# Kernel tuning notes

Measured on AMD Instinct MI355X. Metric: run time of the kernel, lower is better.

Reference implementation:

```python
import jax, jax.numpy as jnp
import numpy as np

HID = 256
E = 2 * HID  # 512, attention embed dim
H = 2        # attention heads


def _lin(x, w, b):
    return x @ w.T + b


def setup_inputs() -> dict:
    key = jax.random.key(0)
    ks = jax.random.split(key, 16)
    N, Ng, G = 65536, 4096, 16
    s = 0.02
    def w(k, o, i):
        return jax.random.normal(k, (o, i), jnp.float32) * s
    return {
        "flat_pair_enc": jax.random.normal(ks[0], (N, E), jnp.float32),
        "flat_pair_encA": jax.random.normal(ks[1], (N, E + 2), jnp.float32),
        "attn_in_w": w(ks[2], 3 * E, E), "attn_in_b": jnp.zeros(3 * E, jnp.float32),
        "attn_out_w": w(ks[3], E, E), "attn_out_b": jnp.zeros(E, jnp.float32),
        "phi1_w1": w(ks[4], HID, E + 2), "phi1_b1": jnp.zeros(HID, jnp.float32),
        "phi1_w2": w(ks[5], HID, HID), "phi1_b2": jnp.zeros(HID, jnp.float32),
        "phi1_w3": w(ks[6], HID, HID), "phi1_b3": jnp.zeros(HID, jnp.float32),
        "phi1_w4": w(ks[7], E, HID), "phi1_b4": jnp.zeros(E, jnp.float32),
        "g_w1": w(ks[8], HID, E), "g_b1": jnp.zeros(HID, jnp.float32),
        "g_w2": w(ks[9], HID, HID), "g_b2": jnp.zeros(HID, jnp.float32),
        "g_w3": w(ks[10], HID, HID), "g_b3": jnp.zeros(HID, jnp.float32),
        "g_w4": w(ks[11], 1, HID), "g_b4": jnp.zeros(1, jnp.float32),
        "phi2_w1": w(ks[12], HID, E), "phi2_b1": jnp.zeros(HID, jnp.float32),
        "phi2_w2": w(ks[13], HID, HID), "phi2_b2": jnp.zeros(HID, jnp.float32),
        "phi2_w3": w(ks[14], 2, HID), "phi2_b3": jnp.zeros(2, jnp.float32),
        "num_groups": 4096,
        "group_size": 16,
    }


def reference(flat_pair_enc, flat_pair_encA,
              attn_in_w, attn_in_b, attn_out_w, attn_out_b,
              phi1_w1, phi1_b1, phi1_w2, phi1_b2, phi1_w3, phi1_b3, phi1_w4, phi1_b4,
              g_w1, g_b1, g_w2, g_b2, g_w3, g_b3, g_w4, g_b4,
              phi2_w1, phi2_b1, phi2_w2, phi2_b2, phi2_w3, phi2_b3,
              num_groups, group_size):
    elu = jax.nn.elu
    Ng, G = num_groups, group_size
    # phi1 (note the double ELU after the second Linear, as in the source)
    h = elu(_lin(flat_pair_encA, phi1_w1, phi1_b1))
    h = elu(elu(_lin(h, phi1_w2, phi1_b2)))
    h = elu(_lin(h, phi1_w3, phi1_b3))
    key1 = _lin(h, phi1_w4, phi1_b4)                      # (N, E)
    x = key1.reshape(Ng, G, E)                            # segmented groups
    # per-group MultiheadAttention (torch semantics: packed in_proj, scale 1/sqrt(dh))
    qkv = x @ attn_in_w.T + attn_in_b                     # (Ng, G, 3E)
    q, k, v = jnp.split(qkv, 3, axis=-1)
    dh = E // H
    def heads(t):
        return t.reshape(Ng, G, H, dh).transpose(0, 2, 1, 3)  # (Ng, H, G, dh)
    q, k, v = heads(q), heads(k), heads(v)
    scores = jnp.einsum('nhqd,nhkd->nhqk', q, k) / jnp.sqrt(jnp.float32(dh))
    a = jax.nn.softmax(scores, axis=-1)
    o = jnp.einsum('nhqk,nhkd->nhqd', a, v).transpose(0, 2, 1, 3).reshape(Ng, G, E)
    key1_mean = (o @ attn_out_w.T + attn_out_b).mean(axis=1)  # (Ng, E) — mean over seq
    # g head
    hg = elu(_lin(key1_mean, g_w1, g_b1))
    hg = elu(_lin(hg, g_w2, g_b2))
    hg = elu(_lin(hg, g_w3, g_b3))
    q_jt = _lin(hg, g_w4, g_b4)                           # (Ng, 1)
    # alt values: k2 + kbar1 - key1/|g|  (counts per group == G)
    alt_val = flat_pair_enc.reshape(Ng, G, E) + key1_mean[:, None, :] - x / G
    hp = elu(_lin(alt_val, phi2_w1, phi2_b1))
    hp = elu(_lin(hp, phi2_w2, phi2_b2))
    alt_q = _lin(hp, phi2_w3, phi2_b3)                    # (Ng, G, 2)
    return (q_jt, alt_q)
```

## Files before the change

### kernel.cpp

```cpp
#include <hip/hip_runtime.h>
#include <cstdint>

typedef __bf16 bf16;
typedef __attribute__((ext_vector_type(8))) __bf16 bf16x8;
typedef __attribute__((ext_vector_type(4))) __bf16 bf16x4;
typedef __attribute__((ext_vector_type(4))) float f32x4;
typedef __attribute__((ext_vector_type(2))) float f32x2;

static __device__ __forceinline__ float elu1(float x) {
    return x > 0.f ? x : (__expf(x) - 1.f);
}

static __device__ __forceinline__ void gl_lds16(const void* gp, void* lp) {
    __builtin_amdgcn_global_load_lds(
        (const __attribute__((address_space(1))) void*)(uintptr_t)gp,
        (__attribute__((address_space(3))) void*)(uint32_t)(uintptr_t)lp,
        16, 0, 0);
}

struct CvtArgs {
    const float* src[13];
    int rows[13];
    int scols[13];
    int dcols[13];
    int total;
};

__global__ void cvt_k(CvtArgs a, bf16* __restrict__ dst) {
    int idx = blockIdx.x * 256 + threadIdx.x;
    if (idx >= a.total) return;
    int rem = idx;
#pragma unroll 1
    for (int s = 0; s < 13; ++s) {
        int sz = a.rows[s] * a.dcols[s];
        if (rem < sz) {
            int r = rem / a.dcols[s];
            int c = rem - r * a.dcols[s];
            float v = (c < a.scols[s]) ? a.src[s][(long)r * a.scols[s] + c] : 0.f;
            dst[idx] = (bf16)v;
            return;
        }
        rem -= sz;
    }
}

struct GemmArgs {
    const float* Af;
    const bf16*  Ab;
    long lda;
    const float* enc;
    const float* km;
    const bf16*  key1;
    const bf16*  W;
    long ldw;
    const float* bias;
    bf16*  Cb;
    float* Cf;
    long ldc;
    int nK;
    int klim;
};

enum { AM_F32 = 0, AM_F32U = 1, AM_BF16 = 2, AM_ALT = 3 };
enum { ACT_NONE = 0, ACT_ELU = 1, ACT_ELU2 = 2 };

template <int AMODE, int ACT, bool OUTB>
__global__ __launch_bounds__(256, 2) void gemm_t(GemmArgs g) {
    __shared__ bf16 As[128 * 64];
    __shared__ bf16 Bs[128 * 64];

    const int tid  = threadIdx.x;
    const int wave = tid >> 6;
    const int lane = tid & 63;
    const int ln   = lane & 15;
    const int quad = lane >> 4;

    const long m0 = (long)blockIdx.x * 128;
    const long n0 = (long)blockIdx.y * 128;
    const int  wm = (wave & 1) * 64;
    const int  wn = (wave >> 1) * 64;

    f32x4 acc[4][4] = {};

    for (int ks = 0; ks < g.nK; ++ks) {
        const int k0 = ks * 64;
        __syncthreads();

        if constexpr (AMODE == AM_BF16) {
            const int cbase = wave * 256;
#pragma unroll
            for (int r = 0; r < 4; ++r) {
                const int c = cbase + r * 64 + lane;
                const int m = c >> 3, s = c & 7;
                const int pg = (s - m) & 7;
                gl_lds16(g.Ab + (m0 + m) * g.lda + k0 + pg * 8, &As[c * 8]);
            }
        } else {
#pragma unroll
            for (int r = 0; r < 4; ++r) {
                const int c = r * 256 + tid;
                const int m = c >> 3, s = c & 7;
                const int pg = (s - m) & 7;
                const int kk = k0 + pg * 8;
                bf16x8 t;
                if constexpr (AMODE == AM_F32) {
                    const float* ap = g.Af + (m0 + m) * g.lda + kk;
                    f32x4 p0 = *(const f32x4*)ap;
                    f32x4 p1 = *(const f32x4*)(ap + 4);
                    t[0] = (bf16)p0.x; t[1] = (bf16)p0.y; t[2] = (bf16)p0.z; t[3] = (bf16)p0.w;
                    t[4] = (bf16)p1.x; t[5] = (bf16)p1.y; t[6] = (bf16)p1.z; t[7] = (bf16)p1.w;
                } else if constexpr (AMODE == AM_F32U) {
                    const float* ap = g.Af + (m0 + m) * g.lda;
                    if (kk + 8 <= g.klim) {
#pragma unroll
                        for (int e = 0; e < 8; e += 2) {
                            f32x2 p = *(const f32x2*)(ap + kk + e);
                            t[e] = (bf16)p.x; t[e + 1] = (bf16)p.y;
                        }
                    } else {
#pragma unroll
                        for (int e = 0; e < 8; ++e) {
                            const int col = kk + e;
                            t[e] = (bf16)(col < g.klim ? ap[col] : 0.f);
                        }
                    }
                } else {
                    const long row = m0 + m;
                    const float* ep = g.enc + row * 512 + kk;
                    const float* mp = g.km + (row >> 4) * 512 + kk;
                    const bf16*  xp = g.key1 + row * 512 + kk;
                    f32x4 e0 = *(const f32x4*)ep;
                    f32x4 e1 = *(const f32x4*)(ep + 4);
                    f32x4 q0 = *(const f32x4*)mp;
                    f32x4 q1 = *(const f32x4*)(mp + 4);
                    bf16x8 x8 = *(const bf16x8*)xp;
                    t[0] = (bf16)(e0.x + q0.x - (float)x8[0] * 0.0625f);
                    t[1] = (bf16)(e0.y + q0.y - (float)x8[1] * 0.0625f);
                    t[2] = (bf16)(e0.z + q0.z - (float)x8[2] * 0.0625f);
                    t[3] = (bf16)(e0.w + q0.w - (float)x8[3] * 0.0625f);
                    t[4] = (bf16)(e1.x + q1.x - (float)x8[4] * 0.0625f);
                    t[5] = (bf16)(e1.y + q1.y - (float)x8[5] * 0.0625f);
                    t[6] = (bf16)(e1.z + q1.z - (float)x8[6] * 0.0625f);
                    t[7] = (bf16)(e1.w + q1.w - (float)x8[7] * 0.0625f);
                }
                *(bf16x8*)(&As[m * 64 + s * 8]) = t;
            }
        }

        {
            const int cbase = wave * 256;
#pragma unroll
            for (int r = 0; r < 4; ++r) {
                const int c = cbase + r * 64 + lane;
                const int n = c >> 3, s = c & 7;
                const int pg = (s - n) & 7;
                gl_lds16(g.W + (n0 + n) * g.ldw + k0 + pg * 8, &Bs[c * 8]);
            }
        }
        __syncthreads();

#pragma unroll
        for (int ksub = 0; ksub < 2; ++ksub) {
            bf16x8 av[4], bv[4];
#pragma unroll
            for (int t = 0; t < 4; ++t) {
                const int m = wm + t * 16 + ln;
                const int sa = ((ksub * 4 + quad) + m) & 7;
                av[t] = *(const bf16x8*)(&As[m * 64 + sa * 8]);
                const int n = wn + t * 16 + ln;
                const int sb = ((ksub * 4 + quad) + n) & 7;
                bv[t] = *(const bf16x8*)(&Bs[n * 64 + sb * 8]);
            }
#pragma unroll
            for (int i = 0; i < 4; ++i)
#pragma unroll
                for (int j = 0; j < 4; ++j)
                    acc[i][j] = __builtin_amdgcn_mfma_f32_16x16x32_bf16(
                        av[i], bv[j], acc[i][j], 0, 0, 0);
        }
    }

#pragma unroll
    for (int i = 0; i < 4; ++i) {
        const long rb = m0 + wm + i * 16 + quad * 4;
#pragma unroll
        for (int j = 0; j < 4; ++j) {
            const long n = n0 + wn + j * 16 + ln;
            const float bvs = g.bias[n];
#pragma unroll
            for (int r = 0; r < 4; ++r) {
                float v = acc[i][j][r] + bvs;
                if constexpr (ACT >= ACT_ELU) v = elu1(v);
                if constexpr (ACT == ACT_ELU2) v = elu1(v);
                const long o = (rb + r) * g.ldc + n;
                if constexpr (OUTB) g.Cb[o] = (bf16)v;
                else                g.Cf[o] = v;
            }
        }
    }
}

__global__ __launch_bounds__(256) void attn_k(const bf16* __restrict__ qkv,
                                              bf16* __restrict__ obar,
                                              int ngroups) {
    const int tid = blockIdx.x * 256 + threadIdx.x;
    const int wv = tid >> 6;
    const int g  = wv >> 1;
    const int h  = wv & 1;
    if (g >= ngroups) return;
    const int lane = threadIdx.x & 63;
    const int i  = lane & 15;
    const int jb = (lane >> 4) << 2;

    const bf16* base  = qkv + (long)g * 16 * 1536;
    const bf16* qrow  = base + (long)i * 1536 + h * 256;
    const bf16* kbase = base + 512 + h * 256;

    float s0 = 0.f, s1 = 0.f, s2 = 0.f, s3 = 0.f;
    for (int kk = 0; kk < 256; kk += 8) {
        bf16x8 qv = *(const bf16x8*)(qrow + kk);
        float qf[8];
#pragma unroll
        for (int e = 0; e < 8; ++e) qf[e] = (float)qv[e];
        bf16x8 k0 = *(const bf16x8*)(kbase + (long)(jb + 0) * 1536 + kk);
        bf16x8 k1 = *(const bf16x8*)(kbase + (long)(jb + 1) * 1536 + kk);
        bf16x8 k2 = *(const bf16x8*)(kbase + (long)(jb + 2) * 1536 + kk);
        bf16x8 k3 = *(const bf16x8*)(kbase + (long)(jb + 3) * 1536 + kk);
#pragma unroll
        for (int e = 0; e < 8; ++e) {
            s0 += qf[e] * (float)k0[e];
            s1 += qf[e] * (float)k1[e];
            s2 += qf[e] * (float)k2[e];
            s3 += qf[e] * (float)k3[e];
        }
    }
    const float sc = 1.f / 16.f;
    s0 *= sc; s1 *= sc; s2 *= sc; s3 *= sc;
    float m = fmaxf(fmaxf(s0, s1), fmaxf(s2, s3));
    m = fmaxf(m, __shfl_xor(m, 16));
    m = fmaxf(m, __shfl_xor(m, 32));
    float e0 = __expf(s0 - m), e1 = __expf(s1 - m), e2 = __expf(s2 - m), e3 = __expf(s3 - m);
    float rs = e0 + e1 + e2 + e3;
    rs += __shfl_xor(rs, 16);
    rs += __shfl_xor(rs, 32);
    const float inv = 1.f / (rs * 16.f);
    float cb[4] = {e0 * inv, e1 * inv, e2 * inv, e3 * inv};
#pragma unroll
    for (int msk = 1; msk <= 8; msk <<= 1) {
        cb[0] += __shfl_xor(cb[0], msk);
        cb[1] += __shfl_xor(cb[1], msk);
        cb[2] += __shfl_xor(cb[2], msk);
        cb[3] += __shfl_xor(cb[3], msk);
    }
    float call[16];
#pragma unroll
    for (int j = 0; j < 16; ++j)
        call[j] = __shfl(cb[j & 3], (j >> 2) << 4);

    const int d0 = lane << 2;
    const bf16* vb = base + 1024 + h * 256 + d0;
    float o0 = 0.f, o1 = 0.f, o2 = 0.f, o3 = 0.f;
#pragma unroll
    for (int j = 0; j < 16; ++j) {
        bf16x4 vv = *(const bf16x4*)(vb + (long)j * 1536);
        o0 += call[j] * (float)vv[0];
        o1 += call[j] * (float)vv[1];
        o2 += call[j] * (float)vv[2];
        o3 += call[j] * (float)vv[3];
    }
    bf16x4 ov;
    ov[0] = (bf16)o0; ov[1] = (bf16)o1; ov[2] = (bf16)o2; ov[3] = (bf16)o3;
    *(bf16x4*)(obar + (long)g * 512 + h * 256 + d0) = ov;
}

__global__ void qjt_k(const bf16* __restrict__ hg, const bf16* __restrict__ w,
                      const float* __restrict__ b, float* __restrict__ out) {
    const int m = blockIdx.x * 256 + threadIdx.x;
    const bf16* hp = hg + (long)m * 256;
    float acc = 0.f;
    for (int k = 0; k < 256; k += 8) {
        bf16x8 hv = *(const bf16x8*)(hp + k);
        bf16x8 wv = *(const bf16x8*)(w + k);
#pragma unroll
        for (int e = 0; e < 8; ++e) acc += (float)hv[e] * (float)wv[e];
    }
    out[m] = acc + b[0];
}

__global__ void altq_k(const bf16* __restrict__ hp, const bf16* __restrict__ w,
                       const float* __restrict__ b, float* __restrict__ out) {
    const int m = blockIdx.x * 256 + threadIdx.x;
    const bf16* hr = hp + (long)m * 256;
    float a0 = 0.f, a1 = 0.f;
    for (int k = 0; k < 256; k += 8) {
        bf16x8 hv = *(const bf16x8*)(hr + k);
        bf16x8 w0 = *(const bf16x8*)(w + k);
        bf16x8 w1 = *(const bf16x8*)(w + 256 + k);
#pragma unroll
        for (int e = 0; e < 8; ++e) {
            float hf = (float)hv[e];
            a0 += hf * (float)w0[e];
            a1 += hf * (float)w1[e];
        }
    }
    out[2 * m]     = a0 + b[0];
    out[2 * m + 1] = a1 + b[1];
}

extern "C" void kernel_launch(void* const* d_in, const int* in_sizes, int n_in,
                              void* d_out, int out_size, void* d_ws, size_t ws_size,
                              hipStream_t stream) {
    const float* enc    = (const float*)d_in[0];
    const float* encA   = (const float*)d_in[1];
    const float* w_ain  = (const float*)d_in[2];
    const float* b_ain  = (const float*)d_in[3];
    const float* w_aout = (const float*)d_in[4];
    const float* b_aout = (const float*)d_in[5];
    const float* w_p11  = (const float*)d_in[6];
    const float* b_p11  = (const float*)d_in[7];
    const float* w_p12  = (const float*)d_in[8];
    const float* b_p12  = (const float*)d_in[9];
    const float* w_p13  = (const float*)d_in[10];
    const float* b_p13  = (const float*)d_in[11];
    const float* w_p14  = (const float*)d_in[12];
    const float* b_p14  = (const float*)d_in[13];
    const float* w_g1   = (const float*)d_in[14];
    const float* b_g1   = (const float*)d_in[15];
    const float* w_g2   = (const float*)d_in[16];
    const float* b_g2   = (const float*)d_in[17];
    const float* w_g3   = (const float*)d_in[18];
    const float* b_g3   = (const float*)d_in[19];
    const float* w_g4   = (const float*)d_in[20];
    const float* b_g4   = (const float*)d_in[21];
    const float* w_p21  = (const float*)d_in[22];
    const float* b_p21  = (const float*)d_in[23];
    const float* w_p22  = (const float*)d_in[24];
    const float* b_p22  = (const float*)d_in[25];
    const float* w_p23  = (const float*)d_in[26];
    const float* b_p23  = (const float*)d_in[27];
    float* out = (float*)d_out;

    char* wsc = (char*)d_ws;
    size_t off = 0;
    auto take = [&](size_t bytes) -> char* {
        char* p = wsc + off;
        off += (bytes + 255) & ~(size_t)255;
        return p;
    };

    const long o_ain  = 0;
    const long o_aout = o_ain + 1536L * 512;
    const long o_p11  = o_aout + 512L * 512;
    const long o_p12  = o_p11 + 256L * 576;
    const long o_p13  = o_p12 + 256L * 256;
    const long o_p14  = o_p13 + 256L * 256;
    const long o_g1   = o_p14 + 512L * 256;
    const long o_g2   = o_g1 + 256L * 512;
    const long o_g3   = o_g2 + 256L * 256;
    const long o_g4   = o_g3 + 256L * 256;
    const long o_p21  = o_g4 + 256L;
    const long o_p22  = o_p21 + 256L * 512;
    const long o_p23  = o_p22 + 256L * 256;
    const long wtot   = o_p23 + 2L * 256;

    bf16*  wb  = (bf16*)take((size_t)wtot * 2);
    bf16*  Ha  = (bf16*)take(65536ull * 256 * 2);
    bf16*  Hb  = (bf16*)take(65536ull * 256 * 2);
    bf16*  K1  = (bf16*)take(65536ull * 512 * 2);
    bf16*  OB  = (bf16*)take(4096ull * 512 * 2);
    float* KM  = (float*)take(4096ull * 512 * 4);
    bf16*  HGa = (bf16*)take(4096ull * 256 * 2);
    bf16*  HGb = (bf16*)take(4096ull * 256 * 2);

    int CH = 16;
    if (off + (65536ull / 2) * 1536 * 2 <= ws_size)      CH = 2;
    else if (off + (65536ull / 4) * 1536 * 2 <= ws_size) CH = 4;
    else if (off + (65536ull / 8) * 1536 * 2 <= ws_size) CH = 8;
    bf16* QKV = (bf16*)take((size_t)(65536 / CH) * 1536 * 2);

    CvtArgs ca;
    const float* srcs[13] = {w_ain, w_aout, w_p11, w_p12, w_p13, w_p14,
                             w_g1, w_g2, w_g3, w_g4, w_p21, w_p22, w_p23};
    const int rows_[13]  = {1536, 512, 256, 256, 256, 512, 256, 256, 256, 1, 256, 256, 2};
    const int scols_[13] = {512, 512, 514, 256, 256, 256, 512, 256, 256, 256, 512, 256, 256};
    const int dcols_[13] = {512, 512, 576, 256, 256, 256, 512, 256, 256, 256, 512, 256, 256};
    for (int s = 0; s < 13; ++s) {
        ca.src[s] = srcs[s]; ca.rows[s] = rows_[s];
        ca.scols[s] = scols_[s]; ca.dcols[s] = dcols_[s];
    }
    ca.total = (int)wtot;
    cvt_k<<<dim3((unsigned)((wtot + 255) / 256)), dim3(256), 0, stream>>>(ca, wb);

    GemmArgs ga;

    ga = {}; ga.Af = encA; ga.lda = 514; ga.klim = 514;
    ga.W = wb + o_p11; ga.ldw = 576; ga.bias = b_p11;
    ga.Cb = Ha; ga.ldc = 256; ga.nK = 9;
    gemm_t<AM_F32U, ACT_ELU, true><<<dim3(512, 2), 256, 0, stream>>>(ga);

    ga = {}; ga.Ab = Ha; ga.lda = 256; ga.W = wb + o_p12; ga.ldw = 256;
    ga.bias = b_p12; ga.Cb = Hb; ga.ldc = 256; ga.nK = 4;
    gemm_t<AM_BF16, ACT_ELU2, true><<<dim3(512, 2), 256, 0, stream>>>(ga);

    ga = {}; ga.Ab = Hb; ga.lda = 256; ga.W = wb + o_p13; ga.ldw = 256;
    ga.bias = b_p13; ga.Cb = Ha; ga.ldc = 256; ga.nK = 4;
    gemm_t<AM_BF16, ACT_ELU, true><<<dim3(512, 2), 256, 0, stream>>>(ga);

    ga = {}; ga.Ab = Ha; ga.lda = 256; ga.W = wb + o_p14; ga.ldw = 256;
    ga.bias = b_p14; ga.Cb = K1; ga.ldc = 512; ga.nK = 4;
    gemm_t<AM_BF16, ACT_NONE, true><<<dim3(512, 4), 256, 0, stream>>>(ga);

    const int Mc = 65536 / CH;
    const int gc = 4096 / CH;
    for (int c = 0; c < CH; ++c) {
        ga = {}; ga.Ab = K1 + (long)c * Mc * 512; ga.lda = 512;
        ga.W = wb + o_ain; ga.ldw = 512; ga.bias = b_ain;
        ga.Cb = QKV; ga.ldc = 1536; ga.nK = 8;
        gemm_t<AM_BF16, ACT_NONE, true>
            <<<dim3(Mc / 128, 12), 256, 0, stream>>>(ga);
        attn_k<<<dim3((gc * 2) / 4), 256, 0, stream>>>(QKV, OB + (long)c * gc * 512, gc);
    }

    ga = {}; ga.Ab = OB; ga.lda = 512; ga.W = wb + o_aout; ga.ldw = 512;
    ga.bias = b_aout; ga.Cf = KM; ga.ldc = 512; ga.nK = 8;
    gemm_t<AM_BF16, ACT_NONE, false><<<dim3(32, 4), 256, 0, stream>>>(ga);

    ga = {}; ga.Af = KM; ga.lda = 512; ga.W = wb + o_g1; ga.ldw = 512;
    ga.bias = b_g1; ga.Cb = HGa; ga.ldc = 256; ga.nK = 8;
    gemm_t<AM_F32, ACT_ELU, true><<<dim3(32, 2), 256, 0, stream>>>(ga);

    ga = {}; ga.Ab = HGa; ga.lda = 256; ga.W = wb + o_g2; ga.ldw = 256;
    ga.bias = b_g2; ga.Cb = HGb; ga.ldc = 256; ga.nK = 4;
    gemm_t<AM_BF16, ACT_ELU, true><<<dim3(32, 2), 256, 0, stream>>>(ga);

    ga = {}; ga.Ab = HGb; ga.lda = 256; ga.W = wb + o_g3; ga.ldw = 256;
    ga.bias = b_g3; ga.Cb = HGa; ga.ldc = 256; ga.nK = 4;
    gemm_t<AM_BF16, ACT_ELU, true><<<dim3(32, 2), 256, 0, stream>>>(ga);

    qjt_k<<<dim3(16), 256, 0, stream>>>(HGa, wb + o_g4, b_g4, out);

    ga = {}; ga.enc = enc; ga.km = KM; ga.key1 = K1;
    ga.W = wb + o_p21; ga.ldw = 512; ga.bias = b_p21;
    ga.Cb = Ha; ga.ldc = 256; ga.nK = 8;
    gemm_t<AM_ALT, ACT_ELU, true><<<dim3(512, 2), 256, 0, stream>>>(ga);

    ga = {}; ga.Ab = Ha; ga.lda = 256; ga.W = wb + o_p22; ga.ldw = 256;
    ga.bias = b_p22; ga.Cb = Hb; ga.ldc = 256; ga.nK = 4;
    gemm_t<AM_BF16, ACT_ELU, true><<<dim3(512, 2), 256, 0, stream>>>(ga);

    altq_k<<<dim3(256), 256, 0, stream>>>(Hb, wb + o_p23, b_p23, out + 4096);
}
```

Measured before the change: 789.3 us.

## Fold V projection into output projection and pre-convert padded encA to bf16

Attention now needs only Q and K from the QKV GEMM. The softmax-weighted average is applied directly to the key1 rows per head. The V projection and the output projection are merged into one precomputed 512x1024 matrix (Mbig), with a constant bias c0 that uses the softmax weights summing to one. This removes a third of the large QKV GEMM's output columns and its memory traffic, at the cost of extra weight-prep kernels and a wider final GEMM. It also converts encA into a padded bf16 buffer once so the first GEMM takes the bf16 path, raises launch bounds to 4 blocks per CU, and tries to use a single chunk (CH=1).

```diff
diff --git a/kernel.cpp b/kernel.cpp
--- a/kernel.cpp
+++ b/kernel.cpp
@@ -42,6 +42,61 @@
         }
         rem -= sz;
     }
+}
+
+__global__ void cvtA_k(const float* __restrict__ src, bf16* __restrict__ dst) {
+    const int idx = blockIdx.x * 256 + threadIdx.x;
+    const int row = idx / 72;
+    const int c0 = (idx - row * 72) * 8;
+    bf16x8 t;
+    if (c0 + 8 <= 514) {
+        const float* p = src + (long)row * 514 + c0;
+#pragma unroll
+        for (int e = 0; e < 8; e += 2) {
+            f32x2 v = *(const f32x2*)(p + e);
+            t[e] = (bf16)v.x; t[e + 1] = (bf16)v.y;
+        }
+    } else if (c0 < 514) {
+        const float* p = src + (long)row * 514;
+#pragma unroll
+        for (int e = 0; e < 8; ++e)
+            t[e] = (bf16)((c0 + e < 514) ? p[c0 + e] : 0.f);
+    } else {
+#pragma unroll
+        for (int e = 0; e < 8; ++e) t[e] = (bf16)0.f;
+    }
+    *(bf16x8*)(dst + (long)row * 576 + c0) = t;
+}
+
+__global__ void mbig_k(const float* __restrict__ w_aout,
+                       const float* __restrict__ w_ain,
+                       bf16* __restrict__ M) {
+    const int n = blockIdx.x;
+    const int tid = threadIdx.x;
+#pragma unroll 1
+    for (int h = 0; h < 2; ++h) {
+#pragma unroll 1
+        for (int kc = 0; kc < 2; ++kc) {
+            const int k = kc * 256 + tid;
+            const float* ao = w_aout + (long)n * 512 + h * 256;
+            const float* ai = w_ain + (long)(1024 + h * 256) * 512 + k;
+            float acc = 0.f;
+#pragma unroll 4
+            for (int d = 0; d < 256; ++d)
+                acc += ao[d] * ai[(long)d * 512];
+            M[(long)n * 1024 + h * 512 + k] = (bf16)acc;
+        }
+    }
+}
+
+__global__ void c0_k(const float* __restrict__ w_aout, const float* __restrict__ bv,
+                     const float* __restrict__ bout, float* __restrict__ c0) {
+    const int n = blockIdx.x * 128 + threadIdx.x;
+    if (n >= 512) return;
+    const float* wr = w_aout + (long)n * 512;
+    float acc = 0.f;
+    for (int d = 0; d < 512; ++d) acc += bv[d] * wr[d];
+    c0[n] = acc + bout[n];
 }
 
 struct GemmArgs {
@@ -58,14 +113,13 @@
     float* Cf;
     long ldc;
     int nK;
-    int klim;
 };
 
-enum { AM_F32 = 0, AM_F32U = 1, AM_BF16 = 2, AM_ALT = 3 };
+enum { AM_F32 = 0, AM_BF16 = 2, AM_ALT = 3 };
 enum { ACT_NONE = 0, ACT_ELU = 1, ACT_ELU2 = 2 };
 
 template <int AMODE, int ACT, bool OUTB>
-__global__ __launch_bounds__(256, 2) void gemm_t(GemmArgs g) {
+__global__ __launch_bounds__(256, 4) void gemm_t(GemmArgs g) {
     __shared__ bf16 As[128 * 64];
     __shared__ bf16 Bs[128 * 64];
 
@@ -109,21 +163,6 @@
                     f32x4 p1 = *(const f32x4*)(ap + 4);
                     t[0] = (bf16)p0.x; t[1] = (bf16)p0.y; t[2] = (bf16)p0.z; t[3] = (bf16)p0.w;
                     t[4] = (bf16)p1.x; t[5] = (bf16)p1.y; t[6] = (bf16)p1.z; t[7] = (bf16)p1.w;
-                } else if constexpr (AMODE == AM_F32U) {
-                    const float* ap = g.Af + (m0 + m) * g.lda;
-                    if (kk + 8 <= g.klim) {
-#pragma unroll
-                        for (int e = 0; e < 8; e += 2) {
-                            f32x2 p = *(const f32x2*)(ap + kk + e);
-                            t[e] = (bf16)p.x; t[e + 1] = (bf16)p.y;
-                        }
-                    } else {
-#pragma unroll
-                        for (int e = 0; e < 8; ++e) {
-                            const int col = kk + e;
-                            t[e] = (bf16)(col < g.klim ? ap[col] : 0.f);
-                        }
-                    }
                 } else {
                     const long row = m0 + m;
                     const float* ep = g.enc + row * 512 + kk;
@@ -200,8 +239,9 @@
     }
 }
 
-__global__ __launch_bounds__(256) void attn_k(const bf16* __restrict__ qkv,
-                                              bf16* __restrict__ obar,
+__global__ __launch_bounds__(256) void attn_k(const bf16* __restrict__ qk,
+                                              const bf16* __restrict__ X,
+                                              bf16* __restrict__ Y,
                                               int ngroups) {
     const int tid = blockIdx.x * 256 + threadIdx.x;
     const int wv = tid >> 6;
@@ -212,8 +252,8 @@
     const int i  = lane & 15;
     const int jb = (lane >> 4) << 2;
 
-    const bf16* base  = qkv + (long)g * 16 * 1536;
-    const bf16* qrow  = base + (long)i * 1536 + h * 256;
+    const bf16* base  = qk + (long)g * 16 * 1024;
+    const bf16* qrow  = base + (long)i * 1024 + h * 256;
     const bf16* kbase = base + 512 + h * 256;
 
     float s0 = 0.f, s1 = 0.f, s2 = 0.f, s3 = 0.f;
@@ -222,10 +262,10 @@
         float qf[8];
 #pragma unroll
         for (int e = 0; e < 8; ++e) qf[e] = (float)qv[e];
-        bf16x8 k0 = *(const bf16x8*)(kbase + (long)(jb + 0) * 1536 + kk);
-        bf16x8 k1 = *(const bf16x8*)(kbase + (long)(jb + 1) * 1536 + kk);
-        bf16x8 k2 = *(const bf16x8*)(kbase + (long)(jb + 2) * 1536 + kk);
-        bf16x8 k3 = *(const bf16x8*)(kbase + (long)(jb + 3) * 1536 + kk);
+        bf16x8 k0 = *(const bf16x8*)(kbase + (long)(jb + 0) * 1024 + kk);
+        bf16x8 k1 = *(const bf16x8*)(kbase + (long)(jb + 1) * 1024 + kk);
+        bf16x8 k2 = *(const bf16x8*)(kbase + (long)(jb + 2) * 1024 + kk);
+        bf16x8 k3 = *(const bf16x8*)(kbase + (long)(jb + 3) * 1024 + kk);
 #pragma unroll
         for (int e = 0; e < 8; ++e) {
             s0 += qf[e] * (float)k0[e];
@@ -257,20 +297,20 @@
     for (int j = 0; j < 16; ++j)
         call[j] = __shfl(cb[j & 3], (j >> 2) << 4);
 
-    const int d0 = lane << 2;
-    const bf16* vb = base + 1024 + h * 256 + d0;
-    float o0 = 0.f, o1 = 0.f, o2 = 0.f, o3 = 0.f;
+    const int c0 = lane << 3;
+    const bf16* xb = X + (long)g * 16 * 512 + c0;
+    float yacc[8] = {};
 #pragma unroll
     for (int j = 0; j < 16; ++j) {
-        bf16x4 vv = *(const bf16x4*)(vb + (long)j * 1536);
-        o0 += call[j] * (float)vv[0];
-        o1 += call[j] * (float)vv[1];
-        o2 += call[j] * (float)vv[2];
-        o3 += call[j] * (float)vv[3];
-    }
-    bf16x4 ov;
-    ov[0] = (bf16)o0; ov[1] = (bf16)o1; ov[2] = (bf16)o2; ov[3] = (bf16)o3;
-    *(bf16x4*)(obar + (long)g * 512 + h * 256 + d0) = ov;
+        bf16x8 xv = *(const bf16x8*)(xb + (long)j * 512);
+        const float cj = call[j];
+#pragma unroll
+        for (int e = 0; e < 8; ++e) yacc[e] += cj * (float)xv[e];
+    }
+    bf16x8 yv;
+#pragma unroll
+    for (int e = 0; e < 8; ++e) yv[e] = (bf16)yacc[e];
+    *(bf16x8*)(Y + (long)g * 1024 + h * 512 + c0) = yv;
 }
 
 __global__ void qjt_k(const bf16* __restrict__ hg, const bf16* __restrict__ w,
@@ -349,8 +389,7 @@
     };
 
     const long o_ain  = 0;
-    const long o_aout = o_ain + 1536L * 512;
-    const long o_p11  = o_aout + 512L * 512;
+    const long o_p11  = o_ain + 1536L * 512;
     const long o_p12  = o_p11 + 256L * 576;
     const long o_p13  = o_p12 + 256L * 256;
     const long o_p14  = o_p13 + 256L * 256;
@@ -361,42 +400,57 @@
     const long o_p21  = o_g4 + 256L;
     const long o_p22  = o_p21 + 256L * 512;
     const long o_p23  = o_p22 + 256L * 256;
-    const long wtot   = o_p23 + 2L * 256;
-
-    bf16*  wb  = (bf16*)take((size_t)wtot * 2);
-    bf16*  Ha  = (bf16*)take(65536ull * 256 * 2);
-    bf16*  Hb  = (bf16*)take(65536ull * 256 * 2);
-    bf16*  K1  = (bf16*)take(65536ull * 512 * 2);
-    bf16*  OB  = (bf16*)take(4096ull * 512 * 2);
-    float* KM  = (float*)take(4096ull * 512 * 4);
-    bf16*  HGa = (bf16*)take(4096ull * 256 * 2);
-    bf16*  HGb = (bf16*)take(4096ull * 256 * 2);
-
+    const long o_aout = o_p23 + 2L * 256;
+    const long wtot   = o_aout + 512L * 512;
+
+    bf16*  wb   = (bf16*)take((size_t)wtot * 2);
+    bf16*  Ha   = (bf16*)take(65536ull * 256 * 2);
+    bf16*  Hb   = (bf16*)take(65536ull * 256 * 2);
+    bf16*  K1   = (bf16*)take(65536ull * 512 * 2);
+    float* KM   = (float*)take(4096ull * 512 * 4);
+    bf16*  HGa  = (bf16*)take(4096ull * 256 * 2);
+    bf16*  HGb  = (bf16*)take(4096ull * 256 * 2);
+    bf16*  Ybig = (bf16*)take(4096ull * 1024 * 2);
+    bf16*  Mbig = (bf16*)take(512ull * 1024 * 2);
+    float* c0v  = (float*)take(512 * 4);
+
+    const size_t acvt_bytes = 65536ull * 576 * 2;
     int CH = 16;
-    if (off + (65536ull / 2) * 1536 * 2 <= ws_size)      CH = 2;
-    else if (off + (65536ull / 4) * 1536 * 2 <= ws_size) CH = 4;
-    else if (off + (65536ull / 8) * 1536 * 2 <= ws_size) CH = 8;
-    bf16* QKV = (bf16*)take((size_t)(65536 / CH) * 1536 * 2);
+    const size_t rem = (ws_size > off) ? ws_size - off : 0;
+    auto fits = [&](int ch) {
+        size_t need = (size_t)(65536 / ch) * 1024 * 2;
+        if (need < acvt_bytes) need = acvt_bytes;
+        return need <= rem;
+    };
+    if (fits(1)) CH = 1;
+    else if (fits(2)) CH = 2;
+    else if (fits(4)) CH = 4;
+    else if (fits(8)) CH = 8;
+    bf16* SHARED = (bf16*)(wsc + off);
+    bf16* Acvt = SHARED;
+    bf16* QK   = SHARED;
 
     CvtArgs ca;
-    const float* srcs[13] = {w_ain, w_aout, w_p11, w_p12, w_p13, w_p14,
-                             w_g1, w_g2, w_g3, w_g4, w_p21, w_p22, w_p23};
-    const int rows_[13]  = {1536, 512, 256, 256, 256, 512, 256, 256, 256, 1, 256, 256, 2};
-    const int scols_[13] = {512, 512, 514, 256, 256, 256, 512, 256, 256, 256, 512, 256, 256};
-    const int dcols_[13] = {512, 512, 576, 256, 256, 256, 512, 256, 256, 256, 512, 256, 256};
+    const float* srcs[13] = {w_ain, w_p11, w_p12, w_p13, w_p14,
+                             w_g1, w_g2, w_g3, w_g4, w_p21, w_p22, w_p23, w_aout};
+    const int rows_[13]  = {1536, 256, 256, 256, 512, 256, 256, 256, 1, 256, 256, 2, 512};
+    const int scols_[13] = {512, 514, 256, 256, 256, 512, 256, 256, 256, 512, 256, 256, 512};
+    const int dcols_[13] = {512, 576, 256, 256, 256, 512, 256, 256, 256, 512, 256, 256, 512};
     for (int s = 0; s < 13; ++s) {
         ca.src[s] = srcs[s]; ca.rows[s] = rows_[s];
         ca.scols[s] = scols_[s]; ca.dcols[s] = dcols_[s];
     }
     ca.total = (int)wtot;
     cvt_k<<<dim3((unsigned)((wtot + 255) / 256)), dim3(256), 0, stream>>>(ca, wb);
+    cvtA_k<<<dim3(65536 * 72 / 256), dim3(256), 0, stream>>>(encA, Acvt);
+    mbig_k<<<dim3(512), dim3(256), 0, stream>>>(w_aout, w_ain, Mbig);
+    c0_k<<<dim3(4), dim3(128), 0, stream>>>(w_aout, b_ain + 1024, b_aout, c0v);
 
     GemmArgs ga;
 
-    ga = {}; ga.Af = encA; ga.lda = 514; ga.klim = 514;
-    ga.W = wb + o_p11; ga.ldw = 576; ga.bias = b_p11;
-    ga.Cb = Ha; ga.ldc = 256; ga.nK = 9;
-    gemm_t<AM_F32U, ACT_ELU, true><<<dim3(512, 2), 256, 0, stream>>>(ga);
+    ga = {}; ga.Ab = Acvt; ga.lda = 576; ga.W = wb + o_p11; ga.ldw = 576;
+    ga.bias = b_p11; ga.Cb = Ha; ga.ldc = 256; ga.nK = 9;
+    gemm_t<AM_BF16, ACT_ELU, true><<<dim3(512, 2), 256, 0, stream>>>(ga);
 
     ga = {}; ga.Ab = Ha; ga.lda = 256; ga.W = wb + o_p12; ga.ldw = 256;
     ga.bias = b_p12; ga.Cb = Hb; ga.ldc = 256; ga.nK = 4;
@@ -415,14 +469,15 @@
     for (int c = 0; c < CH; ++c) {
         ga = {}; ga.Ab = K1 + (long)c * Mc * 512; ga.lda = 512;
         ga.W = wb + o_ain; ga.ldw = 512; ga.bias = b_ain;
-        ga.Cb = QKV; ga.ldc = 1536; ga.nK = 8;
+        ga.Cb = QK; ga.ldc = 1024; ga.nK = 8;
         gemm_t<AM_BF16, ACT_NONE, true>
-            <<<dim3(Mc / 128, 12), 256, 0, stream>>>(ga);
-        attn_k<<<dim3((gc * 2) / 4), 256, 0, stream>>>(QKV, OB + (long)c * gc * 512, gc);
-    }
-
-    ga = {}; ga.Ab = OB; ga.lda = 512; ga.W = wb + o_aout; ga.ldw = 512;
-    ga.bias = b_aout; ga.Cf = KM; ga.ldc = 512; ga.nK = 8;
+            <<<dim3(Mc / 128, 8), 256, 0, stream>>>(ga);
+        attn_k<<<dim3(gc / 2), 256, 0, stream>>>(
+            QK, K1 + (long)c * Mc * 512, Ybig + (long)c * gc * 1024, gc);
+    }
+
+    ga = {}; ga.Ab = Ybig; ga.lda = 1024; ga.W = Mbig; ga.ldw = 1024;
+    ga.bias = c0v; ga.Cf = KM; ga.ldc = 512; ga.nK = 16;
     gemm_t<AM_BF16, ACT_NONE, false><<<dim3(32, 4), 256, 0, stream>>>(ga);
 
     ga = {}; ga.Af = KM; ga.lda = 512; ga.W = wb + o_g1; ga.ldw = 512;
```

Result: slower. 878.5 us (+11.3%).
